# Kernel tuning notes

Hardware: AMD Instinct MI355X
Metric: run time of the kernel (lower is better)

The kernel has to match this reference:

```python
import jax, jax.numpy as jnp
import numpy as np

D = 1024
H = 16
HD = D // H
FF = 4096
B, S = 2, 2048


def _ln(x, g, b, eps):
    mu = jnp.mean(x, axis=-1, keepdims=True)
    var = jnp.mean(jnp.square(x - mu), axis=-1, keepdims=True)
    return (x - mu) * jax.lax.rsqrt(var + eps) * g + b


def setup_inputs() -> dict:
    key = jax.random.key(0)
    ks = jax.random.split(key, 12)
    s = 0.02
    return {
        "x": jax.random.normal(ks[0], (B, S, D), jnp.float32),
        "attention_mask": jnp.ones((B, 1, 1, S), jnp.int32),
        "wq": jax.random.normal(ks[1], (D, D), jnp.float32) * s,
        "bq": jnp.zeros((D,), jnp.float32),
        "wk": jax.random.normal(ks[2], (D, D), jnp.float32) * s,
        "bk": jnp.zeros((D,), jnp.float32),
        "wv": jax.random.normal(ks[3], (D, D), jnp.float32) * s,
        "bv": jnp.zeros((D,), jnp.float32),
        "wo": jax.random.normal(ks[4], (D, D), jnp.float32) * s,
        "bo": jnp.zeros((D,), jnp.float32),
        "ln1_g": jnp.ones((D,), jnp.float32),
        "ln1_b": jnp.zeros((D,), jnp.float32),
        "w1": jax.random.normal(ks[5], (D, FF), jnp.float32) * s,
        "b1": jnp.zeros((FF,), jnp.float32),
        "w2": jax.random.normal(ks[6], (FF, D), jnp.float32) * s,
        "b2": jnp.zeros((D,), jnp.float32),
        "lnf_g": jnp.ones((D,), jnp.float32),
        "lnf_b": jnp.zeros((D,), jnp.float32),
        "ln2_g": jnp.ones((D,), jnp.float32),
        "ln2_b": jnp.zeros((D,), jnp.float32),
    }


def reference(x, attention_mask, wq, bq, wk, bk, wv, bv, wo, bo,
              ln1_g, ln1_b, w1, b1, w2, b2, lnf_g, lnf_b, ln2_g, ln2_b):
    b, s, d = x.shape
    # --- naive multi-head self-attention ---
    q = (x @ wq + bq).reshape(b, s, H, HD).transpose(0, 2, 1, 3)  # [b,h,s,hd]
    k = (x @ wk + bk).reshape(b, s, H, HD).transpose(0, 2, 1, 3)
    v = (x @ wv + bv).reshape(b, s, H, HD).transpose(0, 2, 1, 3)
    scores = jnp.einsum('bhqd,bhkd->bhqk', q, k) / jnp.sqrt(jnp.float32(HD))
    scores = jnp.where(attention_mask == 0, jnp.float32(-1e9), scores)
    attn = jax.nn.softmax(scores, axis=-1)
    ctx = jnp.einsum('bhqk,bhkd->bhqd', attn, v)
    ctx = ctx.transpose(0, 2, 1, 3).reshape(b, s, d)
    attn_out = ctx @ wo + bo
    # residual + LayerNorm (eps=1e-5, torch default)
    x1 = _ln(x + attn_out, ln1_g, ln1_b, 1e-5)
    # --- BERT-style FFN with internal residual LN (eps=1e-12) ---
    h = jax.nn.gelu(x1 @ w1 + b1, approximate=False)
    ff = _ln(h @ w2 + b2 + x1, lnf_g, lnf_b, 1e-12)
    # --- outer residual + LayerNorm (eps=1e-5) ---
    return _ln(x1 + ff, ln2_g, ln2_b, 1e-5)
```

## Files before the change

### kernel.cpp

```cpp
#include <hip/hip_runtime.h>

#define DMODEL 1024
#define NHEAD  16
#define HDIM   64
#define FFDIM  4096
#define BATCH  2
#define SEQ    2048
#define MTOK   (BATCH*SEQ)

typedef __bf16 bf16;
typedef __bf16 bf16x8 __attribute__((ext_vector_type(8)));
typedef __bf16 bf16x4 __attribute__((ext_vector_type(4)));
typedef float  floatx4 __attribute__((ext_vector_type(4)));
typedef unsigned int u32;
typedef unsigned int u32x4 __attribute__((ext_vector_type(4)));

__device__ __forceinline__ int get_flag(const void* ln1g) {
  return (((const u32*)ln1g)[0] == 0x3F800000u) ? 0 : 1;
}
__device__ __forceinline__ float ld_ext(const void* p, size_t i, int flag) {
  return flag ? (float)((const bf16*)p)[i] : ((const float*)p)[i];
}

__device__ __forceinline__ void gload16(const bf16* g, bf16* lds_uniform) {
  __builtin_amdgcn_global_load_lds(
      (const __attribute__((address_space(1))) u32*)g,
      (__attribute__((address_space(3))) u32*)lds_uniform, 16, 0, 0);
}

__device__ __forceinline__ float gelu_f(float v) {
  float e = __expf(-1.702f * v);
  return __fdividef(v, 1.0f + e);
}

__global__ __launch_bounds__(256) void prep(
    const void* wq, const void* wk, const void* wv, const void* wo,
    const void* w1, const void* w2, const void* x, const int* mask,
    bf16* WTqkv, bf16* WToT, bf16* WT1, bf16* WT2, bf16* xC,
    u32* mwAll, bf16* m01All, const void* ln1g)
{
  int flag = get_flag(ln1g);
  int bid = blockIdx.x;
  if (bid >= 16384) {
    int b = bid - 16384;
    int base = b * SEQ + threadIdx.x * 8;
    #pragma unroll
    for (int j = 0; j < 8; j++)
      m01All[base + j] = (bf16)(mask[base + j] ? 1.0f : 0.0f);
    #pragma unroll
    for (int t = 0; t < 4; t++) {
      int k0 = threadIdx.x * 8 + 2 * t;
      u32 mw = (mask[b * SEQ + k0] ? 0x0000FFFFu : 0u) |
               (mask[b * SEQ + k0 + 1] ? 0xFFFF0000u : 0u);
      mwAll[b * (SEQ / 2) + threadIdx.x * 4 + t] = mw;
    }
    return;
  }
  if (bid >= 12288) {
    size_t base = (size_t)(bid - 12288) * 1024;
    int i = threadIdx.x * 4;
    #pragma unroll
    for (int j = 0; j < 4; j++) xC[base + i + j] = (bf16)ld_ext(x, base + i + j, flag);
    return;
  }
  __shared__ bf16 tile[32][33];
  const void* in; bf16* out; int K, N, t;
  if      (bid < 1024)  { in = wq; out = WTqkv;                 K = 1024; N = 1024; t = bid; }
  else if (bid < 2048)  { in = wk; out = WTqkv + 1024 * 1024;   K = 1024; N = 1024; t = bid - 1024; }
  else if (bid < 3072)  { in = wv; out = WTqkv + 2 * 1024 * 1024; K = 1024; N = 1024; t = bid - 2048; }
  else if (bid < 4096)  { in = wo; out = WToT;                  K = 1024; N = 1024; t = bid - 3072; }
  else if (bid < 8192)  { in = w1; out = WT1;                   K = 1024; N = 4096; t = bid - 4096; }
  else                  { in = w2; out = WT2;                   K = 4096; N = 1024; t = bid - 8192; }
  int shift = (N == 4096) ? 7 : 5;
  int k0 = (t >> shift) * 32, n0 = (t & ((1 << shift) - 1)) * 32;
  int tx = threadIdx.x & 31, ty = threadIdx.x >> 5;
  #pragma unroll
  for (int i = ty; i < 32; i += 8)
    tile[i][tx] = (bf16)ld_ext(in, (size_t)(k0 + i) * N + n0 + tx, flag);
  __syncthreads();
  #pragma unroll
  for (int i = ty; i < 32; i += 8)
    out[(size_t)(n0 + i) * K + k0 + tx] = tile[tx][i];
}

__global__ __launch_bounds__(256) void gemm128(
    const bf16* __restrict__ A, const bf16* __restrict__ BT,
    const void* __restrict__ bias0, const void* __restrict__ bias1,
    const void* __restrict__ bias2,
    bf16* __restrict__ out0, bf16* __restrict__ out1, bf16* __restrict__ out2,
    int N, int K, int ksub, int mode, const void* __restrict__ ln1g)
{
  __shared__ __align__(16) char smem[32768];
  bf16* As = (bf16*)smem;
  bf16* Bs = (bf16*)(smem + 16384);
  int flag = get_flag(ln1g);

  int tid = threadIdx.x, lane = tid & 63, w = tid >> 6;
  int wm = w & 1, wn = w >> 1;
  int m0 = blockIdx.x * 128, n0 = blockIdx.y * 128;
  int kstart = blockIdx.z * ksub;
  int r15 = lane & 15, kg = lane >> 4;

  floatx4 acc[4][4];
  #pragma unroll
  for (int mt = 0; mt < 4; mt++)
    #pragma unroll
    for (int nt = 0; nt < 4; nt++) acc[mt][nt] = (floatx4){0.f, 0.f, 0.f, 0.f};

  int srow8 = lane >> 3;
  int skc = (lane & 7) ^ (srow8 & 7);
  const bf16* Ap = A  + (size_t)(m0 + w * 32 + srow8) * K + kstart + skc * 8;
  const bf16* Bp = BT + (size_t)(n0 + w * 32 + srow8) * K + kstart + skc * 8;
  const size_t jstr = (size_t)8 * K;

  for (int it = ksub >> 6; it > 0; it--) {
    #pragma unroll
    for (int j = 0; j < 4; j++) {
      gload16(Ap + j * jstr, As + (size_t)(w * 256 + j * 64) * 8);
      gload16(Bp + j * jstr, Bs + (size_t)(w * 256 + j * 64) * 8);
    }
    Ap += 64; Bp += 64;
    __syncthreads();

    #pragma unroll
    for (int kk = 0; kk < 2; kk++) {
      bf16x8 af[4], bfr[4];
      #pragma unroll
      for (int mt = 0; mt < 4; mt++) {
        int row = wm * 64 + mt * 16 + r15;
        int slot = (kk * 4 + kg) ^ (r15 & 7);
        af[mt] = *(const bf16x8*)&As[(row * 8 + slot) * 8];
      }
      #pragma unroll
      for (int nt = 0; nt < 4; nt++) {
        int row = wn * 64 + nt * 16 + r15;
        int slot = (kk * 4 + kg) ^ (r15 & 7);
        bfr[nt] = *(const bf16x8*)&Bs[(row * 8 + slot) * 8];
      }
      #pragma unroll
      for (int mt = 0; mt < 4; mt++)
        #pragma unroll
        for (int nt = 0; nt < 4; nt++)
          acc[mt][nt] = __builtin_amdgcn_mfma_f32_16x16x32_bf16(af[mt], bfr[nt], acc[mt][nt], 0, 0, 0);
    }
    __syncthreads();
  }

  bf16* scr = (bf16*)(smem + 5120 * w);
  int gcb = n0 + wn * 64;
  int which = (mode == 1) ? (gcb >> 10) : 0;
  int rowg0 = m0 + wm * 64;
  bf16* outp = out0 + (size_t)blockIdx.z * MTOK * N;

  float bvs[4];
  #pragma unroll
  for (int nt = 0; nt < 4; nt++) {
    int gcol = gcb + nt * 16 + r15;
    int bidx = (mode == 1) ? (gcol & 1023) : gcol;
    const void* bp = (mode == 1) ? ((which == 0) ? bias0 : (which == 1) ? bias1 : bias2) : bias0;
    bvs[nt] = (blockIdx.z == 0) ? ld_ext(bp, bidx, flag) : 0.f;
  }

  #pragma unroll
  for (int pass = 0; pass < 2; pass++) {
    #pragma unroll
    for (int mh = 0; mh < 2; mh++) {
      int mt = 2 * pass + mh;
      #pragma unroll
      for (int nt = 0; nt < 4; nt++) {
        int lcol = nt * 16 + r15;
        #pragma unroll
        for (int r = 0; r < 4; r++) {
          int lrow = mh * 16 + kg * 4 + r;
          float val = acc[mt][nt][r] + bvs[nt];
          if (mode == 2) val = gelu_f(val);
          if (mode == 1 && which == 0) val *= 0.125f;
          if (mode == 1 && which == 2) scr[lcol * 40 + lrow] = (bf16)val;
          else                         scr[lrow * 68 + lcol] = (bf16)val;
        }
      }
    }
    if (mode == 1 && which == 2) {
      int hh = (gcb - 2048) >> 6;
      int b = rowg0 >> 11, s0 = rowg0 & 2047;
      #pragma unroll
      for (int it = 0; it < 4; it++) {
        int c = it * 64 + lane;
        int cc = c >> 2, part = c & 3;
        bf16x8 vdat = *(const bf16x8*)&scr[cc * 40 + part * 8];
        *(bf16x8*)(out2 + ((size_t)(b * NHEAD + hh) * HDIM + cc) * SEQ + s0 + pass * 32 + part * 8) = vdat;
      }
    } else {
      #pragma unroll
      for (int it = 0; it < 4; it++) {
        int c = it * 64 + lane;
        int rr = c >> 3, part = c & 7;
        bf16x8 vdat = *(const bf16x8*)&scr[rr * 68 + part * 8];
        int rowg = rowg0 + pass * 32 + rr;
        bf16* dst;
        if (mode == 1) {
          int b = rowg >> 11, s = rowg & 2047;
          int hh = (gcb & 1023) >> 6;
          bf16* o = (which == 0) ? out0 : out1;
          dst = o + ((size_t)(b * NHEAD + hh) * SEQ + s) * HDIM + part * 8;
        } else {
          dst = outp + (size_t)rowg * N + gcb + part * 8;
        }
        *(bf16x8*)dst = vdat;
      }
    }
  }
}

#define VMW(n) asm volatile("s_waitcnt vmcnt(" #n ")" ::: "memory")

#define STAGE_A(dstbuf, koff, qm)                                             \
  { int gch = (lane & 7) ^ (srow8 & 7);                                       \
    _Pragma("unroll") for (int j = 0; j < 2; j++) {                           \
      int rb = (qm) * 64 + j * 128 + w * 8;                                   \
      gload16(A + (size_t)(m0 + rb + srow8) * K + (koff) + gch * 8,           \
              (dstbuf) + (size_t)rb * 64);                                    \
    } }

#define STAGE_B(dstbuf, koff, qn)                                             \
  { int gch = (lane & 7) ^ (srow8 & 7);                                       \
    _Pragma("unroll") for (int j = 0; j < 2; j++) {                           \
      int rb = (2 * j + (w >> 2)) * 64 + (qn) * 32 + (w & 3) * 8;             \
      gload16(BT + (size_t)(n0 + rb + srow8) * K + (koff) + gch * 8,          \
              (dstbuf) + (size_t)rb * 64);                                    \
    } }

#define PHASE(QM, QN, STAGE_STMT, WAIT_STMT)                                  \
  {                                                                           \
    bf16x8 af[4][2], bfr[2][2];                                               \
    _Pragma("unroll") for (int mt = 0; mt < 4; mt++) {                        \
      int row = wm * 128 + (QM) * 64 + mt * 16 + r15;                         \
      _Pragma("unroll") for (int kk = 0; kk < 2; kk++) {                      \
        int slot = (kk * 4 + kg) ^ (r15 & 7);                                 \
        af[mt][kk] = *(const bf16x8*)&Ac[(size_t)(row * 8 + slot) * 8];       \
      }                                                                       \
    }                                                                         \
    _Pragma("unroll") for (int nt = 0; nt < 2; nt++) {                        \
      int row = wn * 64 + (QN) * 32 + nt * 16 + r15;                          \
      _Pragma("unroll") for (int kk = 0; kk < 2; kk++) {                      \
        int slot = (kk * 4 + kg) ^ (r15 & 7);                                 \
        bfr[nt][kk] = *(const bf16x8*)&Bc[(size_t)(row * 8 + slot) * 8];      \
      }                                                                       \
    }                                                                         \
    STAGE_STMT;                                                               \
    WAIT_STMT;                                                                \
    __builtin_amdgcn_s_barrier();                                             \
    asm volatile("" ::: "memory");                                            \
    __builtin_amdgcn_s_setprio(1);                                            \
    _Pragma("unroll") for (int kk = 0; kk < 2; kk++)                          \
      _Pragma("unroll") for (int mt = 0; mt < 4; mt++)                        \
        _Pragma("unroll") for (int nt = 0; nt < 2; nt++)                      \
          acc[(QM) * 4 + mt][(QN) * 2 + nt] =                                 \
              __builtin_amdgcn_mfma_f32_16x16x32_bf16(                        \
                  af[mt][kk], bfr[nt][kk],                                    \
                  acc[(QM) * 4 + mt][(QN) * 2 + nt], 0, 0, 0);                \
    __builtin_amdgcn_s_setprio(0);                                            \
    __builtin_amdgcn_s_barrier();                                             \
    asm volatile("" ::: "memory");                                            \
  }

__global__ __launch_bounds__(512, 2) void gemm256(
    const bf16* __restrict__ A, const bf16* __restrict__ BT,
    const void* __restrict__ bias0, bf16* __restrict__ out0,
    int N, int K, int ksub, int mode, const void* __restrict__ ln1g)
{
  __shared__ __align__(16) char smem[131072];
  int flag = get_flag(ln1g);

  int tid = threadIdx.x, lane = tid & 63, w = tid >> 6;
  int wm = w >> 2, wn = w & 3;
  int r15 = lane & 15, kg = lane >> 4;
  int srow8 = lane >> 3;

  int nx = gridDim.x, ny = gridDim.y;
  int nwg = nx * ny * gridDim.z;
  int wg = blockIdx.x + nx * (blockIdx.y + ny * blockIdx.z);
  if ((nwg & 7) == 0) wg = (wg & 7) * (nwg >> 3) + (wg >> 3);
  int bx = wg % nx, rem = wg / nx;
  int by = rem % ny, bz = rem / ny;

  int m0 = bx * 256, n0 = by * 256;
  int kstart = bz * ksub;
  int NT = ksub >> 6;

  floatx4 acc[8][4];
  #pragma unroll
  for (int mt = 0; mt < 8; mt++)
    #pragma unroll
    for (int nt = 0; nt < 4; nt++) acc[mt][nt] = (floatx4){0.f, 0.f, 0.f, 0.f};

  STAGE_A((bf16*)smem,             kstart, 0);
  STAGE_B((bf16*)(smem + 65536),   kstart, 0);
  STAGE_A((bf16*)smem,             kstart, 1);
  STAGE_B((bf16*)(smem + 65536),   kstart, 1);
  STAGE_A((bf16*)(smem + 32768),   kstart + 64, 0);
  STAGE_B((bf16*)(smem + 98304),   kstart + 64, 0);
  asm volatile("s_waitcnt vmcnt(4)" ::: "memory");
  __builtin_amdgcn_s_barrier();
  asm volatile("" ::: "memory");

  for (int t = 0; t < NT; t++) {
    int cur = (t & 1) * 32768, nxt = ((t + 1) & 1) * 32768;
    bf16* Ac = (bf16*)(smem + cur);
    bf16* Bc = (bf16*)(smem + 65536 + cur);
    bf16* An = (bf16*)(smem + nxt);
    bf16* Bn = (bf16*)(smem + 65536 + nxt);
    int t1 = (t + 1 < NT) ? t + 1 : NT - 1;
    int t2 = (t + 2 < NT) ? t + 2 : NT - 1;
    int k1 = kstart + t1 * 64, k2 = kstart + t2 * 64;
    PHASE(0, 0, STAGE_A(An, k1, 1), VMW(6));
    PHASE(0, 1, STAGE_B(Bn, k1, 1), );
    PHASE(1, 0, STAGE_A(Ac, k2, 0), );
    PHASE(1, 1, STAGE_B(Bc, k2, 0), VMW(8));
  }

  asm volatile("s_waitcnt vmcnt(0)" ::: "memory");
  __builtin_amdgcn_s_barrier();
  asm volatile("" ::: "memory");

  bf16* scr = (bf16*)(smem + 5120 * w);
  int gcb = n0 + wn * 64;
  int rowg0 = m0 + wm * 128;
  bf16* outp = out0 + (size_t)bz * MTOK * (size_t)N;

  float bvs[4];
  #pragma unroll
  for (int nt = 0; nt < 4; nt++) {
    int gcol = gcb + nt * 16 + r15;
    bvs[nt] = (bz == 0) ? ld_ext(bias0, gcol, flag) : 0.f;
  }

  #pragma unroll
  for (int pass = 0; pass < 4; pass++) {
    #pragma unroll
    for (int mh = 0; mh < 2; mh++) {
      int mt = 2 * pass + mh;
      #pragma unroll
      for (int nt = 0; nt < 4; nt++) {
        #pragma unroll
        for (int r = 0; r < 4; r++) {
          int lrow = mh * 16 + kg * 4 + r;
          float val = acc[mt][nt][r] + bvs[nt];
          if (mode == 2) val = gelu_f(val);
          scr[lrow * 68 + nt * 16 + r15] = (bf16)val;
        }
      }
    }
    #pragma unroll
    for (int it = 0; it < 4; it++) {
      int c = it * 64 + lane;
      int rr = c >> 3, part = c & 7;
      bf16x8 vdat = *(const bf16x8*)&scr[rr * 68 + part * 8];
      int rowg = rowg0 + pass * 32 + rr;
      *(bf16x8*)(outp + (size_t)rowg * N + gcb + part * 8) = vdat;
    }
  }
}

__global__ __launch_bounds__(256) void attn_mfma(
    const bf16* __restrict__ q, const bf16* __restrict__ k,
    const bf16* __restrict__ vt, const u32* __restrict__ mwAll,
    const bf16* __restrict__ m01All, bf16* __restrict__ ctx)
{
  __shared__ __align__(16) bf16 Ks[4096];
  __shared__ __align__(16) bf16 Vts[4096];
  __shared__ __align__(16) bf16 Ps[4][2048];

  int tid = threadIdx.x, lane = tid & 63, w = tid >> 6;
  int r15 = lane & 15, kg = lane >> 4;
  int x7 = r15 & 7;
  int bh = blockIdx.x >> 4;
  int qt = blockIdx.x & 15;
  int b = bh >> 4, h = bh & 15;
  int q0 = qt * 128 + w * 32;

  bf16x8 qf[2][2];
  #pragma unroll
  for (int mt = 0; mt < 2; mt++)
    #pragma unroll
    for (int kt2 = 0; kt2 < 2; kt2++)
      qf[mt][kt2] = *(const bf16x8*)(q + ((size_t)bh * SEQ + q0 + mt * 16 + r15) * HDIM + kt2 * 32 + kg * 8);

  floatx4 O[2][4];
  floatx4 lacc[2];
  #pragma unroll
  for (int mt = 0; mt < 2; mt++) {
    lacc[mt] = (floatx4){0.f, 0.f, 0.f, 0.f};
    #pragma unroll
    for (int dt = 0; dt < 4; dt++) O[mt][dt] = (floatx4){0.f, 0.f, 0.f, 0.f};
  }

  int slo = kg ^ x7, shi = (kg + 4) ^ x7;
  const bf16* pap[2][2];
  #pragma unroll
  for (int mt = 0; mt < 2; mt++) {
    pap[mt][0] = &Ps[w][((mt * 16 + r15) * 8 + slo) * 8];
    pap[mt][1] = &Ps[w][((mt * 16 + r15) * 8 + shi) * 8];
  }

  for (int kt = 0; kt < SEQ; kt += 64) {
    #pragma unroll
    for (int j = 0; j < 2; j++) {
      int c = w * 128 + j * 64 + lane;
      int row = c >> 3, cc = c & 7;
      gload16(k + ((size_t)bh * SEQ + kt + row) * HDIM + (cc ^ (row & 7)) * 8,
              Ks + (size_t)(w * 128 + j * 64) * 8);
    }
    #pragma unroll
    for (int j = 0; j < 2; j++) {
      int c = tid + j * 256;
      int row = c >> 3, cc = c & 7;
      u32x4 vv = *(const u32x4*)(vt + ((size_t)bh * HDIM + row) * SEQ + kt + cc * 8);
      u32x4 mw = *(const u32x4*)&mwAll[(size_t)b * (SEQ / 2) + (kt + cc * 8) / 2];
      vv &= mw;
      *(u32x4*)&Vts[(row * 8 + (cc ^ (row & 7))) * 8] = vv;
    }
    __syncthreads();

    floatx4 S[2][4];
    #pragma unroll
    for (int mt = 0; mt < 2; mt++)
      #pragma unroll
      for (int nt = 0; nt < 4; nt++) S[mt][nt] = (floatx4){0.f, 0.f, 0.f, 0.f};
    #pragma unroll
    for (int nt = 0; nt < 4; nt++) {
      int rb = (nt * 16 + r15) * 8;
      bf16x8 kf0 = *(const bf16x8*)&Ks[(rb + slo) * 8];
      bf16x8 kf1 = *(const bf16x8*)&Ks[(rb + shi) * 8];
      #pragma unroll
      for (int mt = 0; mt < 2; mt++) {
        S[mt][nt] = __builtin_amdgcn_mfma_f32_16x16x32_bf16(kf0, qf[mt][0], S[mt][nt], 0, 0, 0);
        S[mt][nt] = __builtin_amdgcn_mfma_f32_16x16x32_bf16(kf1, qf[mt][1], S[mt][nt], 0, 0, 0);
      }
    }

    #pragma unroll
    for (int mt = 0; mt < 2; mt++)
      #pragma unroll
      for (int nt = 0; nt < 4; nt++) {
        bf16x4 pk;
        #pragma unroll
        for (int r = 0; r < 4; r++) pk[r] = (bf16)__expf(S[mt][nt][r]);
        int c2 = 2 * nt + (kg >> 1);
        *(bf16x4*)&Ps[w][((mt * 16 + r15) * 8 + (c2 ^ x7)) * 8 + (kg & 1) * 4] = pk;
      }

    bf16x8 pa[2][2];
    #pragma unroll
    for (int mt = 0; mt < 2; mt++) {
      pa[mt][0] = *(const bf16x8*)pap[mt][0];
      pa[mt][1] = *(const bf16x8*)pap[mt][1];
    }
    bf16x8 m01f0 = *(const bf16x8*)&m01All[(size_t)b * SEQ + kt + kg * 8];
    bf16x8 m01f1 = *(const bf16x8*)&m01All[(size_t)b * SEQ + kt + 32 + kg * 8];
    #pragma unroll
    for (int dt = 0; dt < 4; dt++) {
      int rb = (dt * 16 + r15) * 8;
      bf16x8 vf0 = *(const bf16x8*)&Vts[(rb + slo) * 8];
      bf16x8 vf1 = *(const bf16x8*)&Vts[(rb + shi) * 8];
      #pragma unroll
      for (int mt = 0; mt < 2; mt++) {
        O[mt][dt] = __builtin_amdgcn_mfma_f32_16x16x32_bf16(pa[mt][0], vf0, O[mt][dt], 0, 0, 0);
        O[mt][dt] = __builtin_amdgcn_mfma_f32_16x16x32_bf16(pa[mt][1], vf1, O[mt][dt], 0, 0, 0);
      }
    }
    #pragma unroll
    for (int mt = 0; mt < 2; mt++) {
      lacc[mt] = __builtin_amdgcn_mfma_f32_16x16x32_bf16(pa[mt][0], m01f0, lacc[mt], 0, 0, 0);
      lacc[mt] = __builtin_amdgcn_mfma_f32_16x16x32_bf16(pa[mt][1], m01f1, lacc[mt], 0, 0, 0);
    }
    __syncthreads();
  }

  #pragma unroll
  for (int mt = 0; mt < 2; mt++) {
    float inv[4];
    #pragma unroll
    for (int r = 0; r < 4; r++) inv[r] = 1.f / lacc[mt][r];
    #pragma unroll
    for (int dt = 0; dt < 4; dt++)
      #pragma unroll
      for (int r = 0; r < 4; r++) {
        int srow = q0 + mt * 16 + kg * 4 + r;
        int col = h * 64 + dt * 16 + r15;
        ctx[((size_t)b * SEQ + srow) * DMODEL + col] = (bf16)(O[mt][dt][r] * inv[r]);
      }
  }
}

__global__ __launch_bounds__(256) void ln_kernel(
    const bf16* ba, const bf16* bb, const bf16* bc,
    const void* g, const void* be, float eps, bf16* outb, const void* ln1g)
{
  __shared__ float red1[4], red2[4];
  int flag = get_flag(ln1g);
  size_t base = (size_t)blockIdx.x * DMODEL;
  float v[4];
  #pragma unroll
  for (int i = 0; i < 4; i++) {
    int idx = threadIdx.x + i * 256;
    v[i] = (float)ba[base + idx] + (float)bb[base + idx] + (float)bc[base + idx];
  }
  float sum = v[0] + v[1] + v[2] + v[3];
  #pragma unroll
  for (int o = 32; o > 0; o >>= 1) sum += __shfl_xor(sum, o);
  if ((threadIdx.x & 63) == 0) red1[threadIdx.x >> 6] = sum;
  __syncthreads();
  float mean = (red1[0] + red1[1] + red1[2] + red1[3]) * (1.f / DMODEL);
  float sq = 0.f;
  #pragma unroll
  for (int i = 0; i < 4; i++) { v[i] -= mean; sq += v[i] * v[i]; }
  #pragma unroll
  for (int o = 32; o > 0; o >>= 1) sq += __shfl_xor(sq, o);
  if ((threadIdx.x & 63) == 0) red2[threadIdx.x >> 6] = sq;
  __syncthreads();
  float rstd = rsqrtf((red2[0] + red2[1] + red2[2] + red2[3]) * (1.f / DMODEL) + eps);
  #pragma unroll
  for (int i = 0; i < 4; i++) {
    int idx = threadIdx.x + i * 256;
    outb[base + idx] = (bf16)(v[i] * rstd * ld_ext(g, idx, flag) + ld_ext(be, idx, flag));
  }
}

__global__ __launch_bounds__(256) void ln_double(
    const bf16* p0, const bf16* p1, const bf16* p2, const bf16* p3,
    const bf16* x1,
    const void* gf, const void* bf, const void* g2, const void* b2,
    void* out_ext, const void* ln1g, int np)
{
  __shared__ float red1[4], red2[4];
  int flag = get_flag(ln1g);
  size_t base = (size_t)blockIdx.x * DMODEL;
  float xv[4], v[4];
  #pragma unroll
  for (int i = 0; i < 4; i++) {
    int idx = threadIdx.x + i * 256;
    xv[i] = (float)x1[base + idx];
    v[i] = xv[i] + (float)p0[base + idx] + (float)p1[base + idx];
    if (np == 4) v[i] += (float)p2[base + idx] + (float)p3[base + idx];
  }
  float sum = v[0] + v[1] + v[2] + v[3];
  #pragma unroll
  for (int o = 32; o > 0; o >>= 1) sum += __shfl_xor(sum, o);
  if ((threadIdx.x & 63) == 0) red1[threadIdx.x >> 6] = sum;
  __syncthreads();
  float mean = (red1[0] + red1[1] + red1[2] + red1[3]) * (1.f / DMODEL);
  float sq = 0.f;
  #pragma unroll
  for (int i = 0; i < 4; i++) { v[i] -= mean; sq += v[i] * v[i]; }
  #pragma unroll
  for (int o = 32; o > 0; o >>= 1) sq += __shfl_xor(sq, o);
  if ((threadIdx.x & 63) == 0) red2[threadIdx.x >> 6] = sq;
  __syncthreads();
  float rstd = rsqrtf((red2[0] + red2[1] + red2[2] + red2[3]) * (1.f / DMODEL) + 1e-12f);
  #pragma unroll
  for (int i = 0; i < 4; i++) {
    int idx = threadIdx.x + i * 256;
    float ff = v[i] * rstd * ld_ext(gf, idx, flag) + ld_ext(bf, idx, flag);
    v[i] = xv[i] + (float)(bf16)ff;
  }
  __syncthreads();
  sum = v[0] + v[1] + v[2] + v[3];
  #pragma unroll
  for (int o = 32; o > 0; o >>= 1) sum += __shfl_xor(sum, o);
  if ((threadIdx.x & 63) == 0) red1[threadIdx.x >> 6] = sum;
  __syncthreads();
  mean = (red1[0] + red1[1] + red1[2] + red1[3]) * (1.f / DMODEL);
  sq = 0.f;
  #pragma unroll
  for (int i = 0; i < 4; i++) { v[i] -= mean; sq += v[i] * v[i]; }
  #pragma unroll
  for (int o = 32; o > 0; o >>= 1) sq += __shfl_xor(sq, o);
  if ((threadIdx.x & 63) == 0) red2[threadIdx.x >> 6] = sq;
  __syncthreads();
  rstd = rsqrtf((red2[0] + red2[1] + red2[2] + red2[3]) * (1.f / DMODEL) + 1e-5f);
  #pragma unroll
  for (int i = 0; i < 4; i++) {
    int idx = threadIdx.x + i * 256;
    float y = v[i] * rstd * ld_ext(g2, idx, flag) + ld_ext(b2, idx, flag);
    if (flag) ((bf16*)out_ext)[base + idx] = (bf16)y;
    else      ((float*)out_ext)[base + idx] = y;
  }
}

extern "C" void kernel_launch(void* const* d_in, const int* in_sizes, int n_in,
                              void* d_out, int out_size, void* d_ws, size_t ws_size,
                              hipStream_t stream) {
  const void* x    = d_in[0];
  const int*  msk  = (const int*)d_in[1];
  const void* wq   = d_in[2];
  const void* bq   = d_in[3];
  const void* wk   = d_in[4];
  const void* bk   = d_in[5];
  const void* wv   = d_in[6];
  const void* bv   = d_in[7];
  const void* wo   = d_in[8];
  const void* bo   = d_in[9];
  const void* ln1g = d_in[10];
  const void* ln1b = d_in[11];
  const void* w1   = d_in[12];
  const void* b1   = d_in[13];
  const void* w2   = d_in[14];
  const void* b2   = d_in[15];
  const void* lnfg = d_in[16];
  const void* lnfb = d_in[17];
  const void* ln2g = d_in[18];
  const void* ln2b = d_in[19];

  const size_t MB = 1024 * 1024;
  char* p = (char*)d_ws;
  int big = ws_size >= (size_t)80 * MB;
  bf16* xC     = (bf16*)(p + 0 * MB);
  bf16* qb     = (bf16*)(p + 8 * MB);
  bf16* kb     = (bf16*)(p + 16 * MB);
  bf16* vtb    = (bf16*)(p + 24 * MB);
  bf16* ctxb   = (bf16*)(p + 32 * MB);
  bf16* WTqkv  = (bf16*)(p + 40 * MB);
  bf16* WToT   = (bf16*)(p + 46 * MB);
  bf16* WT1    = (bf16*)(p + 48 * MB);
  bf16* WT2    = (bf16*)(p + (big ? 72 : 56) * MB);
  bf16* ao     = (bf16*)(p + 8 * MB);
  bf16* x1b    = xC;
  bf16* hb     = (bf16*)(p + 8 * MB);
  bf16* ffp    = (bf16*)(p + 40 * MB);
  u32*  mwAll  = (u32*)d_out;
  bf16* m01All = (bf16*)((char*)d_out + 8192);
  const size_t PS = (size_t)MTOK * DMODEL;

  prep<<<16386, 256, 0, stream>>>(wq, wk, wv, wo, w1, w2, x, msk,
                                  WTqkv, WToT, WT1, WT2, xC, mwAll, m01All, ln1g);

  gemm128<<<dim3(MTOK / 128, 3072 / 128, 1), 256, 0, stream>>>(
      xC, WTqkv, bq, bk, bv, qb, kb, vtb, 3072, DMODEL, DMODEL, 1, ln1g);

  attn_mfma<<<BATCH * NHEAD * (SEQ / 128), 256, 0, stream>>>(qb, kb, vtb, mwAll, m01All, ctxb);

  gemm128<<<dim3(MTOK / 128, DMODEL / 128, 2), 256, 0, stream>>>(
      ctxb, WToT, bo, nullptr, nullptr, ao, nullptr, nullptr, DMODEL, DMODEL, 512, 3, ln1g);

  ln_kernel<<<MTOK, 256, 0, stream>>>(ao, ao + PS, xC, ln1g, ln1b,
                                      1e-5f, x1b, ln1g);

  gemm256<<<dim3(MTOK / 256, FFDIM / 256, 1), 512, 0, stream>>>(
      x1b, WT1, b1, hb, FFDIM, DMODEL, DMODEL, 2, ln1g);

  if (big) {
    gemm256<<<dim3(MTOK / 256, DMODEL / 256, 4), 512, 0, stream>>>(
        hb, WT2, b2, ffp, DMODEL, FFDIM, FFDIM / 4, 3, ln1g);
    ln_double<<<MTOK, 256, 0, stream>>>(ffp, ffp + PS, ffp + 2 * PS, ffp + 3 * PS,
                                        x1b, lnfg, lnfb, ln2g, ln2b, d_out, ln1g, 4);
  } else {
    gemm128<<<dim3(MTOK / 128, DMODEL / 128, 2), 256, 0, stream>>>(
        hb, WT2, b2, nullptr, nullptr, ffp, nullptr, nullptr, DMODEL, FFDIM, 2048, 3, ln1g);
    ln_double<<<MTOK, 256, 0, stream>>>(ffp, ffp + PS, ffp, ffp,
                                        x1b, lnfg, lnfb, ln2g, ln2b, d_out, ln1g, 2);
  }
}
```

Before: 369.3 us.

## Double-buffer attention K/V tiles, remap heads, and run QKV projection on gemm256

The attention kernel now double-buffers its K and V^T shared-memory tiles, prefetching the next tile's K via global_load_lds and V/mask into registers while the current tile is computed. This replaces the per-iteration __syncthreads-then-compute pattern with overlapped loads, and adds setprio hints around the MFMA blocks. Block-to-(batch,head) mapping is also changed to interleave heads across blocks. The QKV projection moves from gemm128 to the 256-tile gemm256, which gains a mode-1 epilogue that scatters Q (pre-scaled by 1/8), K and transposed V into per-head layouts. The cost is twice the LDS for K/V in attention and extra epilogue branching in gemm256.

```diff
diff --git a/kernel.cpp b/kernel.cpp
--- a/kernel.cpp
+++ b/kernel.cpp
@@ -32,6 +32,8 @@
   float e = __expf(-1.702f * v);
   return __fdividef(v, 1.0f + e);
 }
+
+#define VMW(n) asm volatile("s_waitcnt vmcnt(" #n ")" ::: "memory")
 
 __global__ __launch_bounds__(256) void prep(
     const void* wq, const void* wk, const void* wv, const void* wo,
@@ -211,8 +213,6 @@
     }
   }
 }
-
-#define VMW(n) asm volatile("s_waitcnt vmcnt(" #n ")" ::: "memory")
 
 #define STAGE_A(dstbuf, koff, qm)                                             \
   { int gch = (lane & 7) ^ (srow8 & 7);                                       \
@@ -266,7 +266,9 @@
 
 __global__ __launch_bounds__(512, 2) void gemm256(
     const bf16* __restrict__ A, const bf16* __restrict__ BT,
-    const void* __restrict__ bias0, bf16* __restrict__ out0,
+    const void* __restrict__ bias0, const void* __restrict__ bias1,
+    const void* __restrict__ bias2,
+    bf16* __restrict__ out0, bf16* __restrict__ out1, bf16* __restrict__ out2,
     int N, int K, int ksub, int mode, const void* __restrict__ ln1g)
 {
   __shared__ __align__(16) char smem[131072];
@@ -325,6 +327,7 @@
 
   bf16* scr = (bf16*)(smem + 5120 * w);
   int gcb = n0 + wn * 64;
+  int which = (mode == 1) ? (gcb >> 10) : 0;
   int rowg0 = m0 + wm * 128;
   bf16* outp = out0 + (size_t)bz * MTOK * (size_t)N;
 
@@ -332,7 +335,9 @@
   #pragma unroll
   for (int nt = 0; nt < 4; nt++) {
     int gcol = gcb + nt * 16 + r15;
-    bvs[nt] = (bz == 0) ? ld_ext(bias0, gcol, flag) : 0.f;
+    int bidx = (mode == 1) ? (gcol & 1023) : gcol;
+    const void* bp = (mode == 1) ? ((which == 0) ? bias0 : (which == 1) ? bias1 : bias2) : bias0;
+    bvs[nt] = (bz == 0) ? ld_ext(bp, bidx, flag) : 0.f;
   }
 
   #pragma unroll
@@ -342,22 +347,46 @@
       int mt = 2 * pass + mh;
       #pragma unroll
       for (int nt = 0; nt < 4; nt++) {
+        int lcol = nt * 16 + r15;
         #pragma unroll
         for (int r = 0; r < 4; r++) {
           int lrow = mh * 16 + kg * 4 + r;
           float val = acc[mt][nt][r] + bvs[nt];
           if (mode == 2) val = gelu_f(val);
-          scr[lrow * 68 + nt * 16 + r15] = (bf16)val;
+          if (mode == 1 && which == 0) val *= 0.125f;
+          if (mode == 1 && which == 2) scr[lcol * 40 + lrow] = (bf16)val;
+          else                         scr[lrow * 68 + lcol] = (bf16)val;
         }
       }
     }
-    #pragma unroll
-    for (int it = 0; it < 4; it++) {
-      int c = it * 64 + lane;
-      int rr = c >> 3, part = c & 7;
-      bf16x8 vdat = *(const bf16x8*)&scr[rr * 68 + part * 8];
-      int rowg = rowg0 + pass * 32 + rr;
-      *(bf16x8*)(outp + (size_t)rowg * N + gcb + part * 8) = vdat;
+    if (mode == 1 && which == 2) {
+      int hh = (gcb - 2048) >> 6;
+      int bb = rowg0 >> 11, s0 = rowg0 & 2047;
+      #pragma unroll
+      for (int it = 0; it < 4; it++) {
+        int c = it * 64 + lane;
+        int cc = c >> 2, part = c & 3;
+        bf16x8 vdat = *(const bf16x8*)&scr[cc * 40 + part * 8];
+        *(bf16x8*)(out2 + ((size_t)(bb * NHEAD + hh) * HDIM + cc) * SEQ + s0 + pass * 32 + part * 8) = vdat;
+      }
+    } else {
+      #pragma unroll
+      for (int it = 0; it < 4; it++) {
+        int c = it * 64 + lane;
+        int rr = c >> 3, part = c & 7;
+        bf16x8 vdat = *(const bf16x8*)&scr[rr * 68 + part * 8];
+        int rowg = rowg0 + pass * 32 + rr;
+        bf16* dst;
+        if (mode == 1) {
+          int bb = rowg >> 11, s = rowg & 2047;
+          int hh = (gcb & 1023) >> 6;
+          bf16* o = (which == 0) ? out0 : out1;
+          dst = o + ((size_t)(bb * NHEAD + hh) * SEQ + s) * HDIM + part * 8;
+        } else {
+          dst = outp + (size_t)rowg * N + gcb + part * 8;
+        }
+        *(bf16x8*)dst = vdat;
+      }
     }
   }
 }
@@ -367,15 +396,15 @@
     const bf16* __restrict__ vt, const u32* __restrict__ mwAll,
     const bf16* __restrict__ m01All, bf16* __restrict__ ctx)
 {
-  __shared__ __align__(16) bf16 Ks[4096];
-  __shared__ __align__(16) bf16 Vts[4096];
+  __shared__ __align__(16) bf16 Ks[2][4096];
+  __shared__ __align__(16) bf16 Vts[2][4096];
   __shared__ __align__(16) bf16 Ps[4][2048];
 
   int tid = threadIdx.x, lane = tid & 63, w = tid >> 6;
   int r15 = lane & 15, kg = lane >> 4;
   int x7 = r15 & 7;
-  int bh = blockIdx.x >> 4;
-  int qt = blockIdx.x & 15;
+  int bh = (blockIdx.x & 7) * 4 + ((blockIdx.x >> 3) >> 4);
+  int qt = (blockIdx.x >> 3) & 15;
   int b = bh >> 4, h = bh & 15;
   int q0 = qt * 128 + w * 32;
 
@@ -403,41 +432,70 @@
     pap[mt][1] = &Ps[w][((mt * 16 + r15) * 8 + shi) * 8];
   }
 
-  for (int kt = 0; kt < SEQ; kt += 64) {
-    #pragma unroll
-    for (int j = 0; j < 2; j++) {
-      int c = w * 128 + j * 64 + lane;
-      int row = c >> 3, cc = c & 7;
-      gload16(k + ((size_t)bh * SEQ + kt + row) * HDIM + (cc ^ (row & 7)) * 8,
-              Ks + (size_t)(w * 128 + j * 64) * 8);
-    }
-    #pragma unroll
-    for (int j = 0; j < 2; j++) {
-      int c = tid + j * 256;
-      int row = c >> 3, cc = c & 7;
-      u32x4 vv = *(const u32x4*)(vt + ((size_t)bh * HDIM + row) * SEQ + kt + cc * 8);
-      u32x4 mw = *(const u32x4*)&mwAll[(size_t)b * (SEQ / 2) + (kt + cc * 8) / 2];
-      vv &= mw;
-      *(u32x4*)&Vts[(row * 8 + (cc ^ (row & 7))) * 8] = vv;
-    }
-    __syncthreads();
+  int kr = lane >> 3, kc = lane & 7;
+  int vrow = tid >> 3, vcc = tid & 7;
+  int vsw = vcc ^ (vrow & 7);
+  const bf16* kb_ = k + (size_t)bh * SEQ * HDIM;
+  const bf16* vb_ = vt + (size_t)bh * HDIM * SEQ;
+  const u32*  mwb = mwAll + (size_t)b * (SEQ / 2);
+  const bf16* m1b = m01All + (size_t)b * SEQ;
+
+  u32x4 pv0 = *(const u32x4*)(vb_ + (size_t)vrow * SEQ + vcc * 8);
+  u32x4 pv1 = *(const u32x4*)(vb_ + (size_t)(vrow + 32) * SEQ + vcc * 8);
+  u32x4 pmw = *(const u32x4*)&mwb[vcc * 4];
+  bf16x8 m0c = *(const bf16x8*)&m1b[kg * 8];
+  bf16x8 m1c = *(const bf16x8*)&m1b[32 + kg * 8];
+  asm volatile("" ::: "memory");
+  #pragma unroll
+  for (int j = 0; j < 2; j++)
+    gload16(kb_ + (size_t)(16 * w + 8 * j + kr) * HDIM + (kc ^ kr) * 8,
+            &Ks[0][0] + (size_t)(w * 128 + j * 64) * 8);
+  VMW(4);
+  pv0 &= pmw; pv1 &= pmw;
+  *(u32x4*)&Vts[0][(vrow * 8 + vsw) * 8] = pv0;
+  *(u32x4*)&Vts[0][((vrow + 32) * 8 + vsw) * 8] = pv1;
+  asm volatile("s_waitcnt lgkmcnt(0)" ::: "memory");
+  __builtin_amdgcn_s_barrier();
+  asm volatile("" ::: "memory");
+
+  for (int t = 0; t < SEQ / 64; t++) {
+    int cur = t & 1, nxt = cur ^ 1;
+    int ktn = (t + 1 < SEQ / 64) ? (t + 1) * 64 : t * 64;
+    u32x4 nv0 = *(const u32x4*)(vb_ + (size_t)vrow * SEQ + ktn + vcc * 8);
+    u32x4 nv1 = *(const u32x4*)(vb_ + (size_t)(vrow + 32) * SEQ + ktn + vcc * 8);
+    u32x4 nmw = *(const u32x4*)&mwb[(ktn + vcc * 8) >> 1];
+    bf16x8 nm0 = *(const bf16x8*)&m1b[ktn + kg * 8];
+    bf16x8 nm1 = *(const bf16x8*)&m1b[ktn + 32 + kg * 8];
+    asm volatile("" ::: "memory");
+    #pragma unroll
+    for (int j = 0; j < 2; j++)
+      gload16(kb_ + (size_t)(ktn + 16 * w + 8 * j + kr) * HDIM + (kc ^ kr) * 8,
+              &Ks[nxt][0] + (size_t)(w * 128 + j * 64) * 8);
+    VMW(7);
+    __builtin_amdgcn_s_barrier();
+    asm volatile("" ::: "memory");
+
+    const bf16* Kc = &Ks[cur][0];
+    const bf16* Vc = &Vts[cur][0];
 
     floatx4 S[2][4];
     #pragma unroll
     for (int mt = 0; mt < 2; mt++)
       #pragma unroll
       for (int nt = 0; nt < 4; nt++) S[mt][nt] = (floatx4){0.f, 0.f, 0.f, 0.f};
+    __builtin_amdgcn_s_setprio(1);
     #pragma unroll
     for (int nt = 0; nt < 4; nt++) {
       int rb = (nt * 16 + r15) * 8;
-      bf16x8 kf0 = *(const bf16x8*)&Ks[(rb + slo) * 8];
-      bf16x8 kf1 = *(const bf16x8*)&Ks[(rb + shi) * 8];
+      bf16x8 kf0 = *(const bf16x8*)&Kc[(rb + slo) * 8];
+      bf16x8 kf1 = *(const bf16x8*)&Kc[(rb + shi) * 8];
       #pragma unroll
       for (int mt = 0; mt < 2; mt++) {
         S[mt][nt] = __builtin_amdgcn_mfma_f32_16x16x32_bf16(kf0, qf[mt][0], S[mt][nt], 0, 0, 0);
         S[mt][nt] = __builtin_amdgcn_mfma_f32_16x16x32_bf16(kf1, qf[mt][1], S[mt][nt], 0, 0, 0);
       }
     }
+    __builtin_amdgcn_s_setprio(0);
 
     #pragma unroll
     for (int mt = 0; mt < 2; mt++)
@@ -456,13 +514,12 @@
       pa[mt][0] = *(const bf16x8*)pap[mt][0];
       pa[mt][1] = *(const bf16x8*)pap[mt][1];
     }
-    bf16x8 m01f0 = *(const bf16x8*)&m01All[(size_t)b * SEQ + kt + kg * 8];
-    bf16x8 m01f1 = *(const bf16x8*)&m01All[(size_t)b * SEQ + kt + 32 + kg * 8];
+    __builtin_amdgcn_s_setprio(1);
     #pragma unroll
     for (int dt = 0; dt < 4; dt++) {
       int rb = (dt * 16 + r15) * 8;
-      bf16x8 vf0 = *(const bf16x8*)&Vts[(rb + slo) * 8];
-      bf16x8 vf1 = *(const bf16x8*)&Vts[(rb + shi) * 8];
+      bf16x8 vf0 = *(const bf16x8*)&Vc[(rb + slo) * 8];
+      bf16x8 vf1 = *(const bf16x8*)&Vc[(rb + shi) * 8];
       #pragma unroll
       for (int mt = 0; mt < 2; mt++) {
         O[mt][dt] = __builtin_amdgcn_mfma_f32_16x16x32_bf16(pa[mt][0], vf0, O[mt][dt], 0, 0, 0);
@@ -471,11 +528,21 @@
     }
     #pragma unroll
     for (int mt = 0; mt < 2; mt++) {
-      lacc[mt] = __builtin_amdgcn_mfma_f32_16x16x32_bf16(pa[mt][0], m01f0, lacc[mt], 0, 0, 0);
-      lacc[mt] = __builtin_amdgcn_mfma_f32_16x16x32_bf16(pa[mt][1], m01f1, lacc[mt], 0, 0, 0);
-    }
-    __syncthreads();
-  }
+      lacc[mt] = __builtin_amdgcn_mfma_f32_16x16x32_bf16(pa[mt][0], m0c, lacc[mt], 0, 0, 0);
+      lacc[mt] = __builtin_amdgcn_mfma_f32_16x16x32_bf16(pa[mt][1], m1c, lacc[mt], 0, 0, 0);
+    }
+    __builtin_amdgcn_s_setprio(0);
+
+    VMW(2);
+    nv0 &= nmw; nv1 &= nmw;
+    *(u32x4*)&Vts[nxt][(vrow * 8 + vsw) * 8] = nv0;
+    *(u32x4*)&Vts[nxt][((vrow + 32) * 8 + vsw) * 8] = nv1;
+    m0c = nm0; m1c = nm1;
+    asm volatile("s_waitcnt lgkmcnt(0)" ::: "memory");
+    __builtin_amdgcn_s_barrier();
+    asm volatile("" ::: "memory");
+  }
+  VMW(0);
 
   #pragma unroll
   for (int mt = 0; mt < 2; mt++) {
@@ -635,7 +702,7 @@
   prep<<<16386, 256, 0, stream>>>(wq, wk, wv, wo, w1, w2, x, msk,
                                   WTqkv, WToT, WT1, WT2, xC, mwAll, m01All, ln1g);
 
-  gemm128<<<dim3(MTOK / 128, 3072 / 128, 1), 256, 0, stream>>>(
+  gemm256<<<dim3(MTOK / 256, 3072 / 256, 1), 512, 0, stream>>>(
       xC, WTqkv, bq, bk, bv, qb, kb, vtb, 3072, DMODEL, DMODEL, 1, ln1g);
 
   attn_mfma<<<BATCH * NHEAD * (SEQ / 128), 256, 0, stream>>>(qb, kb, vtb, mwAll, m01All, ctxb);
@@ -647,11 +714,11 @@
                                       1e-5f, x1b, ln1g);
 
   gemm256<<<dim3(MTOK / 256, FFDIM / 256, 1), 512, 0, stream>>>(
-      x1b, WT1, b1, hb, FFDIM, DMODEL, DMODEL, 2, ln1g);
+      x1b, WT1, b1, nullptr, nullptr, hb, nullptr, nullptr, FFDIM, DMODEL, DMODEL, 2, ln1g);
 
   if (big) {
     gemm256<<<dim3(MTOK / 256, DMODEL / 256, 4), 512, 0, stream>>>(
-        hb, WT2, b2, ffp, DMODEL, FFDIM, FFDIM / 4, 3, ln1g);
+        hb, WT2, b2, nullptr, nullptr, ffp, nullptr, nullptr, DMODEL, FFDIM, FFDIM / 4, 3, ln1g);
     ln_double<<<MTOK, 256, 0, stream>>>(ffp, ffp + PS, ffp + 2 * PS, ffp + 3 * PS,
                                         x1b, lnfg, lnfb, ln2g, ln2b, d_out, ln1g, 4);
   } else {
```

Result: slower. 376.9 us (+2.0%).
